# Optimization experiments

Hardware: AMD Instinct MI355X
Metric: run time of the kernel (lower is better)

Reference implementation:

```python
import jax, jax.numpy as jnp
import numpy as np

B, T, H, W = 2, 4, 32, 32
DINO_DIM, COG_DIM, NUM_HEADS = 768, 1920, 12
HEAD_DIM = DINO_DIM // NUM_HEADS


def _layernorm(x, g, b, eps=1e-5):
    mu = jnp.mean(x, axis=-1, keepdims=True)
    var = jnp.mean(jnp.square(x - mu), axis=-1, keepdims=True)
    return (x - mu) * jax.lax.rsqrt(var + eps) * g + b


def setup_inputs() -> dict:
    key = jax.random.key(0)
    ks = jax.random.split(key, 12)
    s_d = 1.0 / np.sqrt(DINO_DIM)
    s_c = 1.0 / np.sqrt(COG_DIM)
    return {
        "dino_query": jax.random.normal(ks[0], (B, DINO_DIM, H, W), jnp.float32),
        "cogvideo_keys": jax.random.normal(ks[1], (B, T, H, W, COG_DIM), jnp.float32),
        "temporal_weights": jax.random.uniform(ks[2], (T,), jnp.float32),
        "Wq": jax.random.normal(ks[3], (DINO_DIM, DINO_DIM), jnp.float32) * s_d,
        "bq": jnp.zeros((DINO_DIM,), jnp.float32),
        "Wk": jax.random.normal(ks[4], (COG_DIM, DINO_DIM), jnp.float32) * s_c,
        "bk": jnp.zeros((DINO_DIM,), jnp.float32),
        "Wv": jax.random.normal(ks[5], (COG_DIM, DINO_DIM), jnp.float32) * s_c,
        "bv": jnp.zeros((DINO_DIM,), jnp.float32),
        "Wo": jax.random.normal(ks[6], (DINO_DIM, DINO_DIM), jnp.float32) * s_d,
        "bo": jnp.zeros((DINO_DIM,), jnp.float32),
        "gq": jnp.ones((DINO_DIM,), jnp.float32),
        "Bq": jnp.zeros((DINO_DIM,), jnp.float32),
        "gkv": jnp.ones((COG_DIM,), jnp.float32),
        "Bkv": jnp.zeros((COG_DIM,), jnp.float32),
    }


def reference(dino_query, cogvideo_keys, temporal_weights,
              Wq, bq, Wk, bk, Wv, bv, Wo, bo, gq, Bq, gkv, Bkv):
    b, c, h, w = dino_query.shape
    t = cogvideo_keys.shape[1]
    hw, tkv = h * w, t * cogvideo_keys.shape[2] * cogvideo_keys.shape[3]

    # [B,C,H,W] -> [B,H,W,C]; project after LayerNorm
    xq = _layernorm(jnp.transpose(dino_query, (0, 2, 3, 1)), gq, Bq)
    xkv = _layernorm(cogvideo_keys, gkv, Bkv)
    q = xq @ Wq + bq                      # [B,H,W,C]
    k = xkv @ Wk + bk                     # [B,T,Hk,Wk,C]
    v = xkv @ Wv + bv

    q = q.reshape(b, hw, NUM_HEADS, HEAD_DIM).transpose(0, 2, 1, 3)    # [B,nh,HW,hd]
    k = k.reshape(b, tkv, NUM_HEADS, HEAD_DIM).transpose(0, 2, 1, 3)   # [B,nh,TKV,hd]
    v = v.reshape(b, tkv, NUM_HEADS, HEAD_DIM).transpose(0, 2, 1, 3)

    scores = jnp.einsum('bnqd,bnkd->bnqk', q, k) / np.sqrt(HEAD_DIM)   # [B,nh,HW,TKV]
    # per-key temporal weight: each of the T frames contributes HW keys
    w_key = jnp.repeat(temporal_weights, tkv // t)                     # [TKV]
    scores = scores * w_key[None, None, None, :]
    probs = jax.nn.softmax(scores, axis=-1)

    out = jnp.einsum('bnqk,bnkd->bnqd', probs, v)                      # [B,nh,HW,hd]
    out = out.transpose(0, 2, 1, 3).reshape(b, h, w, c)
    out = out @ Wo + bo
    return jnp.transpose(out, (0, 3, 1, 2))                            # [B,C,H,W]
```

## Files before the change

### kernel.cpp

```cpp
#include <hip/hip_runtime.h>
#include <hip/hip_bf16.h>
#include <math.h>

#define BB   2
#define HWl  1024
#define DINO 768
#define COG  1920
#define NHh  12
#define TKV  4096
#define MQ   (BB*HWl)
#define MKV  (BB*TKV)
#define NSPL 4
#define ROWS_PER_SPLIT (BB*NHh*HWl)

typedef __attribute__((ext_vector_type(8))) short bf16x8;
typedef __attribute__((ext_vector_type(4))) float f32x4;

__device__ __forceinline__ unsigned short f2bf_bits(float f) {
    __hip_bfloat16 h = __float2bfloat16(f);
    return *reinterpret_cast<unsigned short*>(&h);
}

__device__ __forceinline__ void glds16(const __hip_bfloat16* g, __hip_bfloat16* l) {
    __builtin_amdgcn_global_load_lds((const __attribute__((address_space(1))) void*)g,
                                     (__attribute__((address_space(3))) void*)l, 16, 0, 0);
}

__global__ __launch_bounds__(256) void prep1(const float* __restrict__ dino,
                                             const float* __restrict__ cog,
                                             const float* __restrict__ gkv, const float* __restrict__ Bkv,
                                             const float* __restrict__ Wq, const float* __restrict__ Wk,
                                             const float* __restrict__ Wv, const float* __restrict__ Wo,
                                             float* __restrict__ xqT,
                                             __hip_bfloat16* __restrict__ xkv,
                                             __hip_bfloat16* WqT, __hip_bfloat16* WkvT, __hip_bfloat16* WoT) {
    int bid = blockIdx.x, tid = threadIdx.x;
    if (bid < 2048) {
        const int W = COG, W4 = W >> 2, NC = 8;
        int row = bid * 4 + (tid >> 6), lane = tid & 63;
        const float4* xr = (const float4*)(cog + (size_t)row * W);
        const float4* g4 = (const float4*)gkv;
        const float4* b4 = (const float4*)Bkv;
        float4 v[NC];
        float s = 0.f, ss = 0.f;
        #pragma unroll
        for (int i = 0; i < NC; ++i) {
            int c = lane + i * 64;
            float4 t = (c < W4) ? xr[c] : (float4){0.f, 0.f, 0.f, 0.f};
            v[i] = t;
            s  += t.x + t.y + t.z + t.w;
            ss += t.x * t.x + t.y * t.y + t.z * t.z + t.w * t.w;
        }
        #pragma unroll
        for (int off = 1; off < 64; off <<= 1) {
            s  += __shfl_xor(s, off);
            ss += __shfl_xor(ss, off);
        }
        float mu = s / W;
        float rstd = rsqrtf(ss / W - mu * mu + 1e-5f);
        ushort4* yr = (ushort4*)(xkv + (size_t)row * W);
        #pragma unroll
        for (int i = 0; i < NC; ++i) {
            int c = lane + i * 64;
            if (c < W4) {
                float4 t = v[i];
                float4 gg = g4[c], bb = b4[c];
                ushort4 o;
                o.x = f2bf_bits((t.x - mu) * rstd * gg.x + bb.x);
                o.y = f2bf_bits((t.y - mu) * rstd * gg.y + bb.y);
                o.z = f2bf_bits((t.z - mu) * rstd * gg.z + bb.z);
                o.w = f2bf_bits((t.w - mu) * rstd * gg.w + bb.w);
                yr[c] = o;
            }
        }
    } else if (bid < 2432) {
        int t = bid - 2048;
        int h0 = (t & 15) * 64;
        int c0 = ((t >> 4) % 12) * 64;
        int b = t / 192;
        __shared__ float T[64][65];
        #pragma unroll
        for (int i = 0; i < 16; ++i) {
            int idx = tid + i * 256;
            int c = idx >> 6, h = idx & 63;
            T[c][h] = dino[((size_t)b * DINO + c0 + c) * HWl + h0 + h];
        }
        __syncthreads();
        #pragma unroll
        for (int i = 0; i < 16; ++i) {
            int idx = tid + i * 256;
            int r = idx >> 6, c = idx & 63;
            xqT[((size_t)b * HWl + h0 + r) * DINO + c0 + c] = T[c][r];
        }
    } else {
        int bid2 = bid - 2432;
        int mid = bid2 / 1440, r = bid2 % 1440;
        int k0 = (r % 60) * 32, n0 = (r / 60) * 32;
        const float* src = (mid == 0) ? Wq : (mid == 1) ? Wk : (mid == 2) ? Wv : Wo;
        __hip_bfloat16* dst;
        int rowoff = 0;
        if (mid == 0) dst = WqT;
        else if (mid == 1) dst = WkvT;
        else if (mid == 2) { dst = WkvT; rowoff = 768; }
        else dst = WoT;
        int K = (mid == 1 || mid == 2) ? COG : DINO;
        if (k0 >= K) return;
        __shared__ float T[32][33];
        #pragma unroll
        for (int i = 0; i < 4; ++i) {
            int idx = tid + i * 256;
            int rr = idx >> 5, c = idx & 31;
            T[rr][c] = src[(size_t)(k0 + rr) * DINO + n0 + c];
        }
        __syncthreads();
        #pragma unroll
        for (int i = 0; i < 4; ++i) {
            int idx = tid + i * 256;
            int rr = idx >> 5, c = idx & 31;
            dst[(size_t)(rowoff + n0 + rr) * K + k0 + c] = __float2bfloat16(T[c][rr]);
        }
    }
}

__global__ __launch_bounds__(256) void prep2(const float* __restrict__ x,
                                             const float* __restrict__ g,
                                             const float* __restrict__ be,
                                             __hip_bfloat16* __restrict__ y) {
    const int W = DINO, NC = 3;
    int row = blockIdx.x * 4 + (threadIdx.x >> 6);
    int lane = threadIdx.x & 63;
    const float4* xr = (const float4*)(x + (size_t)row * W);
    const float4* g4 = (const float4*)g;
    const float4* b4 = (const float4*)be;
    float4 v[NC];
    float s = 0.f, ss = 0.f;
    #pragma unroll
    for (int i = 0; i < NC; ++i) {
        int c = lane + i * 64;
        float4 t = xr[c];
        v[i] = t;
        s  += t.x + t.y + t.z + t.w;
        ss += t.x * t.x + t.y * t.y + t.z * t.z + t.w * t.w;
    }
    #pragma unroll
    for (int off = 1; off < 64; off <<= 1) {
        s  += __shfl_xor(s, off);
        ss += __shfl_xor(ss, off);
    }
    float mu = s / W;
    float rstd = rsqrtf(ss / W - mu * mu + 1e-5f);
    ushort4* yr = (ushort4*)(y + (size_t)row * W);
    #pragma unroll
    for (int i = 0; i < NC; ++i) {
        int c = lane + i * 64;
        float4 t = v[i];
        float4 gg = g4[c], bb = b4[c];
        ushort4 o;
        o.x = f2bf_bits((t.x - mu) * rstd * gg.x + bb.x);
        o.y = f2bf_bits((t.y - mu) * rstd * gg.y + bb.y);
        o.z = f2bf_bits((t.z - mu) * rstd * gg.z + bb.z);
        o.w = f2bf_bits((t.w - mu) * rstd * gg.w + bb.w);
        yr[c] = o;
    }
}

#define VM8 asm volatile("s_waitcnt vmcnt(8)" ::: "memory")
#define VM2 asm volatile("s_waitcnt vmcnt(2)" ::: "memory")
#define VM0 asm volatile("s_waitcnt vmcnt(0)" ::: "memory")
#define SBAR0 __builtin_amdgcn_sched_barrier(0)

#define STAGE_A(d, h, tau) do { \
    int _o = (aRow + (h) * 64) * Kd + (tau) * 64 + cgo; \
    __hip_bfloat16* _dp = SM + (d) * 32768 + (h) * 8192 + wido; \
    glds16(Ag + _o, _dp); \
    glds16(Ag + _o + 128 * Kd, _dp + 4096); \
} while (0)

#define STAGE_B(d, h, tau) do { \
    int _o = (bRow + (h) * 32) * Kd + (tau) * 64 + cgo; \
    __hip_bfloat16* _dp = SM + (d) * 32768 + 16384 + (h) * 8192 + wido; \
    glds16(Bg + _o, _dp); \
    glds16(Bg + _o + 128 * Kd, _dp + 4096); \
} while (0)

#define LDS_A_FRAG(dst, MH) do { \
    const __hip_bfloat16* _Ab = SM + cur * 32768 + (MH) * 8192 + aoff; \
    _Pragma("unroll") \
    for (int i = 0; i < 4; ++i) { \
        dst[i][0] = *(const bf16x8*)(_Ab + i * 1024 + c0); \
        dst[i][1] = *(const bf16x8*)(_Ab + i * 1024 + c1); \
    } \
} while (0)

#define LDS_B_FRAG(dst, NH) do { \
    const __hip_bfloat16* _Bb = SM + cur * 32768 + 16384 + (NH) * 8192 + boff; \
    _Pragma("unroll") \
    for (int j = 0; j < 2; ++j) { \
        dst[j][0] = *(const bf16x8*)(_Bb + j * 1024 + c0); \
        dst[j][1] = *(const bf16x8*)(_Bb + j * 1024 + c1); \
    } \
} while (0)

#define MFMA_HALF(MH, af) do { \
    __builtin_amdgcn_s_setprio(1); \
    _Pragma("unroll") \
    for (int i = 0; i < 4; ++i) \
        _Pragma("unroll") \
        for (int j = 0; j < 2; ++j) { \
            f32x4 _t = acc[(MH) * 4 + i][j]; \
            _t = __builtin_amdgcn_mfma_f32_16x16x32_bf16(af[i][0], b0[j][0], _t, 0, 0, 0); \
            _t = __builtin_amdgcn_mfma_f32_16x16x32_bf16(af[i][1], b0[j][1], _t, 0, 0, 0); \
            acc[(MH) * 4 + i][j] = _t; \
        } \
    _Pragma("unroll") \
    for (int i = 0; i < 4; ++i) \
        _Pragma("unroll") \
        for (int j = 0; j < 2; ++j) { \
            f32x4 _t = acc[(MH) * 4 + i][2 + j]; \
            _t = __builtin_amdgcn_mfma_f32_16x16x32_bf16(af[i][0], b1[j][0], _t, 0, 0, 0); \
            _t = __builtin_amdgcn_mfma_f32_16x16x32_bf16(af[i][1], b1[j][1], _t, 0, 0, 0); \
            acc[(MH) * 4 + i][2 + j] = _t; \
        } \
    __builtin_amdgcn_s_setprio(0); \
} while (0)

__global__ __launch_bounds__(512, 2) void stage1(const __hip_bfloat16* __restrict__ xq,
                                                 const __hip_bfloat16* __restrict__ WqT,
                                                 const float* __restrict__ bq,
                                                 __hip_bfloat16* __restrict__ qb,
                                                 const __hip_bfloat16* __restrict__ xkv,
                                                 const __hip_bfloat16* __restrict__ WkvT,
                                                 const float* __restrict__ bk,
                                                 const float* __restrict__ bv,
                                                 __hip_bfloat16* __restrict__ kb,
                                                 __hip_bfloat16* __restrict__ VT) {
    __shared__ __hip_bfloat16 SM[65536];
    int bid = blockIdx.x;
    int tid = threadIdx.x;
    int wid = tid >> 6, lane = tid & 63;
    int l4 = lane & 15, lq = lane >> 4;
    int wr = wid >> 2, wc = wid & 3;
    int tr = tid >> 3;
    int cgo = ((tid & 7) ^ (tr & 7)) * 8;
    int wido = wid * 512;

    const __hip_bfloat16 *Ag, *Bg;
    int m0, n0, Kd, NT, isQ;
    if (bid < 192) {
        int x = bid & 7, i = bid >> 3;
        m0 = (x * 4 + (i & 3)) * 256; n0 = (i >> 2) * 256;
        Ag = xkv; Bg = WkvT; Kd = COG; NT = COG / 64; isQ = 0;
    } else {
        int t = bid - 192;
        m0 = (t & 7) * 256; n0 = (t >> 3) * 256;
        Ag = xq; Bg = WqT; Kd = DINO; NT = DINO / 64; isQ = 1;
    }

    const int aRow = m0 + tr;
    const int bRow = n0 + ((tid >> 8) << 6) + (tr & 31);
    const int aoff = (wr * 64 + l4) * 64;
    const int boff = (wc * 32 + l4) * 64;
    const int c0 = ((lq) ^ (l4 & 7)) * 8;
    const int c1 = ((4 + lq) ^ (l4 & 7)) * 8;

    f32x4 acc[8][4];
    #pragma unroll
    for (int i = 0; i < 8; ++i)
        #pragma unroll
        for (int j = 0; j < 4; ++j) acc[i][j] = (f32x4){0.f, 0.f, 0.f, 0.f};

    bf16x8 a0[4][2], a1[4][2], b0[2][2], b1[2][2];

    STAGE_A(0, 0, 0); STAGE_B(0, 0, 0); STAGE_B(0, 1, 0); STAGE_A(0, 1, 0);

    for (int g = 0; g < NT; ++g) {
        int cur = g & 1, nxt = cur ^ 1;
        bool s1 = (g + 1 < NT);
        if (s1) { STAGE_A(nxt, 0, g + 1); STAGE_B(nxt, 0, g + 1); STAGE_B(nxt, 1, g + 1); VM8; }
        else VM2;
        SBAR0; __builtin_amdgcn_s_barrier(); SBAR0;
        LDS_A_FRAG(a0, 0);
        LDS_B_FRAG(b0, 0);
        LDS_B_FRAG(b1, 1);
        MFMA_HALF(0, a0);
        if (s1) { STAGE_A(nxt, 1, g + 1); VM8; }
        else VM0;
        SBAR0; __builtin_amdgcn_s_barrier(); SBAR0;
        LDS_A_FRAG(a1, 1);
        MFMA_HALF(1, a1);
    }

    if (isQ) {
        #pragma unroll
        for (int ii = 0; ii < 8; ++ii)
            #pragma unroll
            for (int jj = 0; jj < 4; ++jj) {
                int m = m0 + wr * 128 + (ii >> 2) * 64 + (ii & 3) * 16 + lq * 4;
                int n = n0 + wc * 64 + (jj >> 1) * 32 + (jj & 1) * 16 + l4;
                float bb = bq[n];
                #pragma unroll
                for (int r = 0; r < 4; ++r)
                    qb[(size_t)(m + r) * DINO + n] = __float2bfloat16(acc[ii][jj][r] + bb);
            }
    } else if (n0 < 768) {
        #pragma unroll
        for (int ii = 0; ii < 8; ++ii)
            #pragma unroll
            for (int jj = 0; jj < 4; ++jj) {
                int m = m0 + wr * 128 + (ii >> 2) * 64 + (ii & 3) * 16 + lq * 4;
                int n = n0 + wc * 64 + (jj >> 1) * 32 + (jj & 1) * 16 + l4;
                float bb = bk[n];
                #pragma unroll
                for (int r = 0; r < 4; ++r)
                    kb[(size_t)(m + r) * DINO + n] = __float2bfloat16(acc[ii][jj][r] + bb);
            }
    } else {
        #pragma unroll
        for (int ii = 0; ii < 8; ++ii)
            #pragma unroll
            for (int jj = 0; jj < 4; ++jj) {
                int m = m0 + wr * 128 + (ii >> 2) * 64 + (ii & 3) * 16 + lq * 4;
                int nv = n0 - 768 + wc * 64 + (jj >> 1) * 32 + (jj & 1) * 16 + l4;
                float bb = bv[nv];
                ushort4 pk;
                pk.x = f2bf_bits(acc[ii][jj][0] + bb);
                pk.y = f2bf_bits(acc[ii][jj][1] + bb);
                pk.z = f2bf_bits(acc[ii][jj][2] + bb);
                pk.w = f2bf_bits(acc[ii][jj][3] + bb);
                *(ushort4*)&VT[((size_t)((m >> 12) * 768 + nv)) * TKV + (m & 4095)] = pk;
            }
    }
}

__global__ __launch_bounds__(256) void gemm_o(const __hip_bfloat16* __restrict__ A,
                                              const __hip_bfloat16* __restrict__ Bt,
                                              const float* __restrict__ bias,
                                              float* __restrict__ out) {
    const int K = DINO;
    __shared__ __hip_bfloat16 As[64 * 64];
    __shared__ __hip_bfloat16 Bs[64 * 64];
    int m0 = blockIdx.x * 64, n0 = blockIdx.y * 64;
    int tid = threadIdx.x, w = tid >> 6, lane = tid & 63;
    int l4 = lane & 15, lq = lane >> 4;
    int mq = (w & 1) * 32, nq = (w >> 1) * 32;
    f32x4 acc[2][2];
    #pragma unroll
    for (int i = 0; i < 2; ++i)
        #pragma unroll
        for (int j = 0; j < 2; ++j) acc[i][j] = (f32x4){0.f, 0.f, 0.f, 0.f};

    int rr = tid >> 3;
    int gc = (tid & 7) ^ (rr & 7);
    const __hip_bfloat16* ag = A  + (size_t)(m0 + rr) * K + gc * 8;
    const __hip_bfloat16* bg = Bt + (size_t)(n0 + rr) * K + gc * 8;
    __hip_bfloat16* asl = As + (w * 8) * 64;
    __hip_bfloat16* bsl = Bs + (w * 8) * 64;
    int sws = l4 & 7;

    for (int k0 = 0; k0 < K; k0 += 64) {
        __syncthreads();
        #pragma unroll
        for (int g = 0; g < 2; ++g) {
            glds16(ag + (size_t)(g * 32) * K + k0, asl + g * 32 * 64);
            glds16(bg + (size_t)(g * 32) * K + k0, bsl + g * 32 * 64);
        }
        __syncthreads();
        #pragma unroll
        for (int h = 0; h < 2; ++h) {
            bf16x8 a[2], b[2];
            #pragma unroll
            for (int i = 0; i < 2; ++i)
                a[i] = *(const bf16x8*)(As + (mq + 16 * i + l4) * 64 + (((h * 4 + lq) ^ sws) * 8));
            #pragma unroll
            for (int j = 0; j < 2; ++j)
                b[j] = *(const bf16x8*)(Bs + (nq + 16 * j + l4) * 64 + (((h * 4 + lq) ^ sws) * 8));
            #pragma unroll
            for (int i = 0; i < 2; ++i)
                #pragma unroll
                for (int j = 0; j < 2; ++j)
                    acc[i][j] = __builtin_amdgcn_mfma_f32_16x16x32_bf16(b[j], a[i], acc[i][j], 0, 0, 0);
        }
    }
    #pragma unroll
    for (int i = 0; i < 2; ++i)
        #pragma unroll
        for (int j = 0; j < 2; ++j)
            #pragma unroll
            for (int r = 0; r < 4; ++r) {
                int n = n0 + nq + 16 * j + lq * 4 + r;
                int m = m0 + mq + 16 * i + l4;
                int b = m >> 10, hw = m & 1023;
                out[((size_t)b * DINO + n) * HWl + hw] = acc[i][j][r] + bias[n];
            }
}

__global__ __launch_bounds__(256) void attn4(const __hip_bfloat16* __restrict__ qb,
                                             const __hip_bfloat16* __restrict__ kb,
                                             const __hip_bfloat16* __restrict__ VT,
                                             const float* __restrict__ tw,
                                             __hip_bfloat16* __restrict__ Opart,
                                             float* __restrict__ lpart) {
    int bid = blockIdx.x;
    int g = bid % 96, qc = bid / 96;
    int s = g & 3, bh = g >> 2;
    int head = bh % NHh, b = bh / NHh;
    int tid = threadIdx.x, w = tid >> 6, lane = tid & 63;
    int l4 = lane & 15, lq = lane >> 4;

    __shared__ __hip_bfloat16 Ks[2 * 64 * 64];
    __shared__ __hip_bfloat16 Vs[2 * 64 * 64];
    __shared__ __hip_bfloat16 Ps[4 * 32 * 64];

    const __hip_bfloat16* qbase = qb + (size_t)(b * HWl + qc * 128 + w * 32 + l4) * DINO + head * 64;
    bf16x8 qA0 = *(const bf16x8*)(qbase + lq * 8);
    bf16x8 qA1 = *(const bf16x8*)(qbase + 32 + lq * 8);
    const __hip_bfloat16* qbase2 = qbase + (size_t)16 * DINO;
    bf16x8 qB0 = *(const bf16x8*)(qbase2 + lq * 8);
    bf16x8 qB1 = *(const bf16x8*)(qbase2 + 32 + lq * 8);

    float c = tw[s] * 0.125f * 1.44269504f;
    float l_iA = 0.f, l_iB = 0.f;
    f32x4 oA[4], oB[4];
    #pragma unroll
    for (int j = 0; j < 4; ++j) { oA[j] = (f32x4){0.f,0.f,0.f,0.f}; oB[j] = (f32x4){0.f,0.f,0.f,0.f}; }

    int rowA = w * 16 + (lane >> 3);
    int cg = (lane & 7) ^ ((lane >> 3) & 7);
    const __hip_bfloat16* kg0 = kb + (size_t)(b * TKV + s * 1024 + rowA) * DINO + head * 64 + cg * 8;
    const __hip_bfloat16* kg1 = kg0 + (size_t)8 * DINO;
    const __hip_bfloat16* vg0 = VT + (size_t)(b * 768 + head * 64 + rowA) * TKV + s * 1024 + cg * 8;
    const __hip_bfloat16* vg1 = vg0 + (size_t)8 * TKV;
    int klo0 = (w * 2 + 0) * 512, klo1 = (w * 2 + 1) * 512;

    int sw0 = (lq ^ (l4 & 7)) * 8;
    int sw1 = ((4 + lq) ^ (l4 & 7)) * 8;
    __hip_bfloat16* PsA = Ps + w * 2048 + l4 * 64;
    __hip_bfloat16* PsB = Ps + w * 2048 + (16 + l4) * 64;

    glds16(kg0, Ks + klo0);
    glds16(kg1, Ks + klo1);
    glds16(vg0, Vs + klo0);
    glds16(vg1, Vs + klo1);

    for (int kt = 0; kt < 16; ++kt) {
        int cur = (kt & 1) * 4096;
        __syncthreads();
        if (kt < 15) {
            int nxt = cur ^ 4096;
            glds16(kg0 + (size_t)(kt + 1) * 64 * DINO, Ks + nxt + klo0);
            glds16(kg1 + (size_t)(kt + 1) * 64 * DINO, Ks + nxt + klo1);
            glds16(vg0 + (kt + 1) * 64, Vs + nxt + klo0);
            glds16(vg1 + (kt + 1) * 64, Vs + nxt + klo1);
        }
        const __hip_bfloat16* Kc = Ks + cur;
        const __hip_bfloat16* Vc = Vs + cur;

        f32x4 stA[4], stB[4];
        #pragma unroll
        for (int j = 0; j < 4; ++j) {
            const __hip_bfloat16* kr = Kc + (16 * j + l4) * 64;
            bf16x8 kf0 = *(const bf16x8*)(kr + sw0);
            bf16x8 kf1 = *(const bf16x8*)(kr + sw1);
            f32x4 a = (f32x4){0.f,0.f,0.f,0.f};
            a = __builtin_amdgcn_mfma_f32_16x16x32_bf16(kf0, qA0, a, 0, 0, 0);
            a = __builtin_amdgcn_mfma_f32_16x16x32_bf16(kf1, qA1, a, 0, 0, 0);
            stA[j] = a;
            f32x4 bb = (f32x4){0.f,0.f,0.f,0.f};
            bb = __builtin_amdgcn_mfma_f32_16x16x32_bf16(kf0, qB0, bb, 0, 0, 0);
            bb = __builtin_amdgcn_mfma_f32_16x16x32_bf16(kf1, qB1, bb, 0, 0, 0);
            stB[j] = bb;
        }

        float lsA = 0.f, lsB = 0.f;
        #pragma unroll
        for (int j = 0; j < 4; ++j)
            #pragma unroll
            for (int r = 0; r < 4; ++r) {
                float eA = exp2f(stA[j][r] * c);
                float eB = exp2f(stB[j][r] * c);
                stA[j][r] = eA; lsA += eA;
                stB[j][r] = eB; lsB += eB;
            }
        lsA += __shfl_xor(lsA, 16); lsA += __shfl_xor(lsA, 32);
        lsB += __shfl_xor(lsB, 16); lsB += __shfl_xor(lsB, 32);
        l_iA += lsA; l_iB += lsB;

        #pragma unroll
        for (int j = 0; j < 4; ++j) {
            int off = (((2 * j + (lq >> 1)) ^ (l4 & 7)) << 3) + (lq & 1) * 4;
            ushort4 pA, pB;
            pA.x = f2bf_bits(stA[j][0]); pA.y = f2bf_bits(stA[j][1]);
            pA.z = f2bf_bits(stA[j][2]); pA.w = f2bf_bits(stA[j][3]);
            pB.x = f2bf_bits(stB[j][0]); pB.y = f2bf_bits(stB[j][1]);
            pB.z = f2bf_bits(stB[j][2]); pB.w = f2bf_bits(stB[j][3]);
            *(ushort4*)&PsA[off] = pA;
            *(ushort4*)&PsB[off] = pB;
        }
        bf16x8 paA0 = *(const bf16x8*)(PsA + sw0);
        bf16x8 paA1 = *(const bf16x8*)(PsA + sw1);
        bf16x8 paB0 = *(const bf16x8*)(PsB + sw0);
        bf16x8 paB1 = *(const bf16x8*)(PsB + sw1);

        #pragma unroll
        for (int j = 0; j < 4; ++j) {
            const __hip_bfloat16* vr = Vc + (16 * j + l4) * 64;
            bf16x8 vf0 = *(const bf16x8*)(vr + sw0);
            bf16x8 vf1 = *(const bf16x8*)(vr + sw1);
            oA[j] = __builtin_amdgcn_mfma_f32_16x16x32_bf16(paA0, vf0, oA[j], 0, 0, 0);
            oA[j] = __builtin_amdgcn_mfma_f32_16x16x32_bf16(paA1, vf1, oA[j], 0, 0, 0);
            oB[j] = __builtin_amdgcn_mfma_f32_16x16x32_bf16(paB0, vf0, oB[j], 0, 0, 0);
            oB[j] = __builtin_amdgcn_mfma_f32_16x16x32_bf16(paB1, vf1, oB[j], 0, 0, 0);
        }
    }

    size_t rb = (size_t)s * ROWS_PER_SPLIT + (size_t)(b * NHh + head) * HWl + qc * 128 + w * 32;
    #pragma unroll
    for (int j = 0; j < 4; ++j)
        #pragma unroll
        for (int r = 0; r < 4; ++r) {
            Opart[(rb + lq * 4 + r) * 64 + j * 16 + l4]      = __float2bfloat16(oA[j][r]);
            Opart[(rb + 16 + lq * 4 + r) * 64 + j * 16 + l4] = __float2bfloat16(oB[j][r]);
        }
    if (lq == 0) {
        lpart[rb + l4]      = l_iA;
        lpart[rb + 16 + l4] = l_iB;
    }
}

__global__ void combine(const __hip_bfloat16* __restrict__ Opart, const float* __restrict__ lpart,
                        __hip_bfloat16* __restrict__ attn) {
    int p = blockIdx.x * 4 + (threadIdx.x >> 6);
    int d = threadIdx.x & 63;
    float L = 0.f, O = 0.f;
    #pragma unroll
    for (int s = 0; s < NSPL; ++s) {
        L += lpart[(size_t)s * ROWS_PER_SPLIT + p];
        O += __bfloat162float(Opart[((size_t)s * ROWS_PER_SPLIT + p) * 64 + d]);
    }
    float res = O / L;
    int q = p & 1023;
    int bh = p >> 10;
    int head = bh % NHh, b = bh / NHh;
    attn[((size_t)(b * HWl + q)) * DINO + head * 64 + d] = __float2bfloat16(res);
}

extern "C" void kernel_launch(void* const* d_in, const int* in_sizes, int n_in,
                              void* d_out, int out_size, void* d_ws, size_t ws_size,
                              hipStream_t stream) {
    (void)in_sizes; (void)n_in; (void)out_size; (void)ws_size;
    const float* dino = (const float*)d_in[0];
    const float* cog  = (const float*)d_in[1];
    const float* tw   = (const float*)d_in[2];
    const float* Wq   = (const float*)d_in[3];
    const float* bq   = (const float*)d_in[4];
    const float* Wk   = (const float*)d_in[5];
    const float* bk   = (const float*)d_in[6];
    const float* Wv   = (const float*)d_in[7];
    const float* bv   = (const float*)d_in[8];
    const float* Wo   = (const float*)d_in[9];
    const float* bo   = (const float*)d_in[10];
    const float* gq   = (const float*)d_in[11];
    const float* Bq   = (const float*)d_in[12];
    const float* gkv  = (const float*)d_in[13];
    const float* Bkv  = (const float*)d_in[14];

    char* p = (char*)d_ws;
    float* xqT = (float*)p;                    p += (size_t)MQ * DINO * 4;
    __hip_bfloat16* xq = (__hip_bfloat16*)p;   p += (size_t)MQ * DINO * 2;
    char* alias = p;                           p += (size_t)MKV * COG * 2;
    __hip_bfloat16* xkv = (__hip_bfloat16*)alias;
    __hip_bfloat16* WqT  = (__hip_bfloat16*)p; p += (size_t)DINO * DINO * 2;
    __hip_bfloat16* WkvT = (__hip_bfloat16*)p; p += (size_t)1536 * COG * 2;
    __hip_bfloat16* WoT  = (__hip_bfloat16*)p; p += (size_t)DINO * DINO * 2;
    __hip_bfloat16* qb   = (__hip_bfloat16*)p; p += (size_t)MQ  * DINO * 2;
    __hip_bfloat16* kb   = (__hip_bfloat16*)p; p += (size_t)MKV * DINO * 2;
    __hip_bfloat16* VT   = (__hip_bfloat16*)p; p += (size_t)MKV * DINO * 2;
    __hip_bfloat16* attnb = (__hip_bfloat16*)p; p += (size_t)MQ * DINO * 2;
    __hip_bfloat16* Opart = (__hip_bfloat16*)alias;
    float* lpart = (float*)(alias + (size_t)NSPL * ROWS_PER_SPLIT * 64 * 2);

    prep1<<<8192, 256, 0, stream>>>(dino, cog, gkv, Bkv,
                                    Wq, Wk, Wv, Wo, xqT, xkv, WqT, WkvT, WoT);
    prep2<<<MQ / 4, 256, 0, stream>>>(xqT, gq, Bq, xq);
    stage1<<<216, 512, 0, stream>>>(xq, WqT, bq, qb, xkv, WkvT, bk, bv, kb, VT);
    attn4<<<BB * NHh * 8 * NSPL, 256, 0, stream>>>(qb, kb, VT, tw, Opart, lpart);
    combine<<<ROWS_PER_SPLIT / 4, 256, 0, stream>>>(Opart, lpart, attnb);
    gemm_o<<<dim3(32, 12), 256, 0, stream>>>(attnb, WoT, bo, (float*)d_out);
}
```

Baseline: 255.6 us.

## Fuse split-K attention combine into output projection GEMM; simplify stage1 pipeline waits

Removes the separate combine kernel and attn buffer. gemm_o now reads the four split partial outputs and row sums, normalizes them and writes the bf16 A tile straight into shared memory before the MFMA loop. This saves a launch and a round trip of the attention output through global memory. The cost is that each of the 12 column blocks recomputes the combine for its rows, and A loads become synchronous register loads instead of async LDS loads. Separately, the stage1 GEMM main loop now does a full vmcnt(0) wait with one barrier per iteration and issues all next-stage loads together, replacing the finer-grained two-barrier pipelining.

```diff
diff --git a/kernel.cpp b/kernel.cpp
--- a/kernel.cpp
+++ b/kernel.cpp
@@ -164,8 +164,6 @@
     }
 }
 
-#define VM8 asm volatile("s_waitcnt vmcnt(8)" ::: "memory")
-#define VM2 asm volatile("s_waitcnt vmcnt(2)" ::: "memory")
 #define VM0 asm volatile("s_waitcnt vmcnt(0)" ::: "memory")
 #define SBAR0 __builtin_amdgcn_sched_barrier(0)
 
@@ -276,16 +274,16 @@
     for (int g = 0; g < NT; ++g) {
         int cur = g & 1, nxt = cur ^ 1;
         bool s1 = (g + 1 < NT);
-        if (s1) { STAGE_A(nxt, 0, g + 1); STAGE_B(nxt, 0, g + 1); STAGE_B(nxt, 1, g + 1); VM8; }
-        else VM2;
+        VM0;
         SBAR0; __builtin_amdgcn_s_barrier(); SBAR0;
+        if (s1) {
+            STAGE_A(nxt, 0, g + 1); STAGE_B(nxt, 0, g + 1);
+            STAGE_B(nxt, 1, g + 1); STAGE_A(nxt, 1, g + 1);
+        }
         LDS_A_FRAG(a0, 0);
         LDS_B_FRAG(b0, 0);
         LDS_B_FRAG(b1, 1);
         MFMA_HALF(0, a0);
-        if (s1) { STAGE_A(nxt, 1, g + 1); VM8; }
-        else VM0;
-        SBAR0; __builtin_amdgcn_s_barrier(); SBAR0;
         LDS_A_FRAG(a1, 1);
         MFMA_HALF(1, a1);
     }
@@ -332,7 +330,8 @@
     }
 }
 
-__global__ __launch_bounds__(256) void gemm_o(const __hip_bfloat16* __restrict__ A,
+__global__ __launch_bounds__(256) void gemm_o(const __hip_bfloat16* __restrict__ Opart,
+                                              const float* __restrict__ lpart,
                                               const __hip_bfloat16* __restrict__ Bt,
                                               const float* __restrict__ bias,
                                               float* __restrict__ out) {
@@ -351,29 +350,76 @@
 
     int rr = tid >> 3;
     int gc = (tid & 7) ^ (rr & 7);
-    const __hip_bfloat16* ag = A  + (size_t)(m0 + rr) * K + gc * 8;
     const __hip_bfloat16* bg = Bt + (size_t)(n0 + rr) * K + gc * 8;
-    __hip_bfloat16* asl = As + (w * 8) * 64;
     __hip_bfloat16* bsl = Bs + (w * 8) * 64;
     int sws = l4 & 7;
 
+    int bq_ = m0 >> 10;
+    int q0 = m0 & 1023;
+    int ar = tid >> 2;
+    int dg = tid & 3;
+    size_t abase = (size_t)(bq_ * NHh) * HWl + q0 + ar;
+
     for (int k0 = 0; k0 < K; k0 += 64) {
         __syncthreads();
-        #pragma unroll
-        for (int g = 0; g < 2; ++g) {
-            glds16(ag + (size_t)(g * 32) * K + k0, asl + g * 32 * 64);
+        int h = k0 >> 6;
+        size_t rowb = abase + (size_t)h * HWl;
+        float o[16];
+        #pragma unroll
+        for (int e = 0; e < 16; ++e) o[e] = 0.f;
+        float L = 0.f;
+        #pragma unroll
+        for (int s = 0; s < NSPL; ++s) {
+            size_t rb = (size_t)s * ROWS_PER_SPLIT + rowb;
+            const ushort4* op = (const ushort4*)(Opart + rb * 64 + dg * 16);
+            ushort4 u0 = op[0], u1 = op[1], u2 = op[2], u3 = op[3];
+            o[0]  += __bfloat162float(*(const __hip_bfloat16*)&u0.x);
+            o[1]  += __bfloat162float(*(const __hip_bfloat16*)&u0.y);
+            o[2]  += __bfloat162float(*(const __hip_bfloat16*)&u0.z);
+            o[3]  += __bfloat162float(*(const __hip_bfloat16*)&u0.w);
+            o[4]  += __bfloat162float(*(const __hip_bfloat16*)&u1.x);
+            o[5]  += __bfloat162float(*(const __hip_bfloat16*)&u1.y);
+            o[6]  += __bfloat162float(*(const __hip_bfloat16*)&u1.z);
+            o[7]  += __bfloat162float(*(const __hip_bfloat16*)&u1.w);
+            o[8]  += __bfloat162float(*(const __hip_bfloat16*)&u2.x);
+            o[9]  += __bfloat162float(*(const __hip_bfloat16*)&u2.y);
+            o[10] += __bfloat162float(*(const __hip_bfloat16*)&u2.z);
+            o[11] += __bfloat162float(*(const __hip_bfloat16*)&u2.w);
+            o[12] += __bfloat162float(*(const __hip_bfloat16*)&u3.x);
+            o[13] += __bfloat162float(*(const __hip_bfloat16*)&u3.y);
+            o[14] += __bfloat162float(*(const __hip_bfloat16*)&u3.z);
+            o[15] += __bfloat162float(*(const __hip_bfloat16*)&u3.w);
+            L += lpart[rb];
+        }
+        float rinv = 1.f / L;
+        ushort4 w0, w1, w2, w3;
+        w0.x = f2bf_bits(o[0] * rinv);  w0.y = f2bf_bits(o[1] * rinv);
+        w0.z = f2bf_bits(o[2] * rinv);  w0.w = f2bf_bits(o[3] * rinv);
+        w1.x = f2bf_bits(o[4] * rinv);  w1.y = f2bf_bits(o[5] * rinv);
+        w1.z = f2bf_bits(o[6] * rinv);  w1.w = f2bf_bits(o[7] * rinv);
+        w2.x = f2bf_bits(o[8] * rinv);  w2.y = f2bf_bits(o[9] * rinv);
+        w2.z = f2bf_bits(o[10] * rinv); w2.w = f2bf_bits(o[11] * rinv);
+        w3.x = f2bf_bits(o[12] * rinv); w3.y = f2bf_bits(o[13] * rinv);
+        w3.z = f2bf_bits(o[14] * rinv); w3.w = f2bf_bits(o[15] * rinv);
+        int g0 = ((dg * 2) ^ (ar & 7)) * 8;
+        int g1 = ((dg * 2 + 1) ^ (ar & 7)) * 8;
+        *(ushort4*)&As[ar * 64 + g0]     = w0;
+        *(ushort4*)&As[ar * 64 + g0 + 4] = w1;
+        *(ushort4*)&As[ar * 64 + g1]     = w2;
+        *(ushort4*)&As[ar * 64 + g1 + 4] = w3;
+        #pragma unroll
+        for (int g = 0; g < 2; ++g)
             glds16(bg + (size_t)(g * 32) * K + k0, bsl + g * 32 * 64);
-        }
         __syncthreads();
         #pragma unroll
-        for (int h = 0; h < 2; ++h) {
+        for (int hh = 0; hh < 2; ++hh) {
             bf16x8 a[2], b[2];
             #pragma unroll
             for (int i = 0; i < 2; ++i)
-                a[i] = *(const bf16x8*)(As + (mq + 16 * i + l4) * 64 + (((h * 4 + lq) ^ sws) * 8));
+                a[i] = *(const bf16x8*)(As + (mq + 16 * i + l4) * 64 + (((hh * 4 + lq) ^ sws) * 8));
             #pragma unroll
             for (int j = 0; j < 2; ++j)
-                b[j] = *(const bf16x8*)(Bs + (nq + 16 * j + l4) * 64 + (((h * 4 + lq) ^ sws) * 8));
+                b[j] = *(const bf16x8*)(Bs + (nq + 16 * j + l4) * 64 + (((hh * 4 + lq) ^ sws) * 8));
             #pragma unroll
             for (int i = 0; i < 2; ++i)
                 #pragma unroll
@@ -525,23 +571,6 @@
         lpart[rb + l4]      = l_iA;
         lpart[rb + 16 + l4] = l_iB;
     }
-}
-
-__global__ void combine(const __hip_bfloat16* __restrict__ Opart, const float* __restrict__ lpart,
-                        __hip_bfloat16* __restrict__ attn) {
-    int p = blockIdx.x * 4 + (threadIdx.x >> 6);
-    int d = threadIdx.x & 63;
-    float L = 0.f, O = 0.f;
-    #pragma unroll
-    for (int s = 0; s < NSPL; ++s) {
-        L += lpart[(size_t)s * ROWS_PER_SPLIT + p];
-        O += __bfloat162float(Opart[((size_t)s * ROWS_PER_SPLIT + p) * 64 + d]);
-    }
-    float res = O / L;
-    int q = p & 1023;
-    int bh = p >> 10;
-    int head = bh % NHh, b = bh / NHh;
-    attn[((size_t)(b * HWl + q)) * DINO + head * 64 + d] = __float2bfloat16(res);
 }
 
 extern "C" void kernel_launch(void* const* d_in, const int* in_sizes, int n_in,
@@ -575,7 +604,6 @@
     __hip_bfloat16* qb   = (__hip_bfloat16*)p; p += (size_t)MQ  * DINO * 2;
     __hip_bfloat16* kb   = (__hip_bfloat16*)p; p += (size_t)MKV * DINO * 2;
     __hip_bfloat16* VT   = (__hip_bfloat16*)p; p += (size_t)MKV * DINO * 2;
-    __hip_bfloat16* attnb = (__hip_bfloat16*)p; p += (size_t)MQ * DINO * 2;
     __hip_bfloat16* Opart = (__hip_bfloat16*)alias;
     float* lpart = (float*)(alias + (size_t)NSPL * ROWS_PER_SPLIT * 64 * 2);
 
@@ -584,6 +612,5 @@
     prep2<<<MQ / 4, 256, 0, stream>>>(xqT, gq, Bq, xq);
     stage1<<<216, 512, 0, stream>>>(xq, WqT, bq, qb, xkv, WkvT, bk, bv, kb, VT);
     attn4<<<BB * NHh * 8 * NSPL, 256, 0, stream>>>(qb, kb, VT, tw, Opart, lpart);
-    combine<<<ROWS_PER_SPLIT / 4, 256, 0, stream>>>(Opart, lpart, attnb);
-    gemm_o<<<dim3(32, 12), 256, 0, stream>>>(attnb, WoT, bo, (float*)d_out);
-}
+    gemm_o<<<dim3(32, 12), 256, 0, stream>>>(Opart, lpart, WoT, bo, (float*)d_out);
+}
```

Result: no change. 259.8 us (+1.6%).
